# Kernel tuning notes

Hardware: AMD Instinct MI355X
Metric: run time of the kernel (lower is better)

## Reference

```python
import jax, jax.numpy as jnp
import numpy as np

NUM_NODES = 100000
NUM_EDGES = 1600000
NUM_GRAPHS = 64
IN_DIM, HID, NCLS = 64, 128, 10


def setup_inputs() -> dict:
    key = jax.random.key(0)
    ks = jax.random.split(key, 12)
    x = jax.random.normal(ks[0], (NUM_NODES, IN_DIM), dtype=jnp.float32)
    src = jax.random.randint(ks[1], (NUM_EDGES,), 0, NUM_NODES, dtype=jnp.int32)
    dst = jax.random.randint(ks[2], (NUM_EDGES,), 0, NUM_NODES, dtype=jnp.int32)
    batch = jnp.sort(jax.random.randint(ks[3], (NUM_NODES,), 0, NUM_GRAPHS, dtype=jnp.int32))
    def glorot(k, shape):
        lim = (6.0 / (shape[0] + shape[1])) ** 0.5
        return jax.random.uniform(k, shape, jnp.float32, -lim, lim)
    return {
        "x": x, "src": src, "dst": dst, "batch": batch,
        "W1": glorot(ks[4], (IN_DIM, HID)), "b1": jnp.zeros((HID,), jnp.float32),
        "W2": glorot(ks[5], (HID, HID)), "b2": jnp.zeros((HID,), jnp.float32),
        "Wl1": glorot(ks[6], (HID, HID // 2)), "bl1": jnp.zeros((HID // 2,), jnp.float32),
        "Wl2": glorot(ks[7], (HID // 2, NCLS)), "bl2": jnp.zeros((NCLS,), jnp.float32),
    }


def gcn_conv(x, W, b, src, dst):
    # GCNConv: out = D^{-1/2} (A + I) D^{-1/2} (x @ W) + b, deg from A+I
    h = x @ W  # [N, H]
    ones = jnp.ones((src.shape[0],), h.dtype)
    deg = jax.ops.segment_sum(ones, dst, num_segments=NUM_NODES) + 1.0  # +1 self-loop
    dinv = jax.lax.rsqrt(deg)  # [N]
    norm = dinv[src] * dinv[dst]  # [E]
    msg = h[src] * norm[:, None]  # [E, H] gather + scale
    agg = jax.ops.segment_sum(msg, dst, num_segments=NUM_NODES)  # scatter-add
    agg = agg + h * (dinv * dinv)[:, None]  # self-loop message
    return agg + b


def reference(x, src, dst, batch, W1, b1, W2, b2, Wl1, bl1, Wl2, bl2):
    h = jax.nn.relu(gcn_conv(x, W1, b1, src, dst))
    h = jax.nn.relu(gcn_conv(h, W2, b2, src, dst))
    # global mean pool per graph
    sums = jax.ops.segment_sum(h, batch, num_segments=NUM_GRAPHS)  # [G, H]
    cnts = jax.ops.segment_sum(jnp.ones((h.shape[0],), h.dtype), batch, num_segments=NUM_GRAPHS)
    pooled = sums / jnp.maximum(cnts, 1.0)[:, None]
    h = jax.nn.relu(pooled @ Wl1 + bl1)
    return h @ Wl2 + bl2  # [G, num_classes]
```

## Files before the change

### kernel.cpp

```cpp
#include <hip/hip_runtime.h>
#include <hip/hip_bf16.h>

#define NODES_N 100000
#define EDGES_E 1600000
#define GRAPHS_G 64

#define BIN_SHIFT 7
#define BIN_NODES 128
#define NBINS 782
#define NB1 1024
#define EPB1 1563

typedef unsigned int uint;
typedef unsigned short ushort;
typedef __attribute__((ext_vector_type(8))) short bf16x8;
typedef __attribute__((ext_vector_type(4))) float f32x4;


__device__ inline uint pack_bf2(float lo, float hi) {
    __hip_bfloat162 h2 = __float22bfloat162_rn(make_float2(lo, hi));
    return *reinterpret_cast<uint*>(&h2);
}

__device__ inline void acc_bf2(uint w, float& a0, float& a1) {
    a0 += __uint_as_float(w << 16);
    a1 += __uint_as_float(w & 0xffff0000u);
}

__device__ inline ushort f2bf(float v) {
    __hip_bfloat16 b = __float2bfloat16(v);
    return *reinterpret_cast<ushort*>(&b);
}


__global__ __launch_bounds__(256) void p1_hist_k(const int* __restrict__ dst,
                                                 int* __restrict__ hist_t) {
    __shared__ int h[NBINS];
    for (int i = threadIdx.x; i < NBINS; i += 256) h[i] = 0;
    __syncthreads();
    int b = blockIdx.x;
    int e0 = b * EPB1, e1 = min(EDGES_E, e0 + EPB1);
    for (int e = e0 + threadIdx.x; e < e1; e += 256)
        atomicAdd(&h[dst[e] >> BIN_SHIFT], 1);
    __syncthreads();
    for (int i = threadIdx.x; i < NBINS; i += 256)
        hist_t[i * NB1 + b] = h[i];
}

__global__ __launch_bounds__(256) void p1_scanbins_k(int* __restrict__ hist_t,
                                                     int* __restrict__ bintot) {
    __shared__ int sd[256];
    __shared__ int carry;
    int bin = blockIdx.x, t = threadIdx.x;
    if (t == 0) carry = 0;
    __syncthreads();
    int* row = hist_t + bin * NB1;
    for (int base = 0; base < NB1; base += 256) {
        int v = row[base + t];
        sd[t] = v; __syncthreads();
        for (int o = 1; o < 256; o <<= 1) {
            int x = (t >= o) ? sd[t - o] : 0;
            __syncthreads();
            sd[t] += x;
            __syncthreads();
        }
        row[base + t] = carry + sd[t] - v;
        __syncthreads();
        if (t == 255) carry += sd[255];
        __syncthreads();
    }
    if (t == 0) bintot[bin] = carry;
}

__global__ __launch_bounds__(256) void binstart_k(const int* __restrict__ bintot,
                                                  int* __restrict__ binstart,
                                                  int* __restrict__ rowptr) {
    __shared__ int sd[256];
    __shared__ int carry;
    int t = threadIdx.x;
    if (t == 0) carry = 0;
    __syncthreads();
    for (int base = 0; base < NBINS; base += 256) {
        int i = base + t;
        int v = (i < NBINS) ? bintot[i] : 0;
        sd[t] = v; __syncthreads();
        for (int o = 1; o < 256; o <<= 1) {
            int x = (t >= o) ? sd[t - o] : 0;
            __syncthreads();
            sd[t] += x;
            __syncthreads();
        }
        if (i < NBINS) binstart[i] = carry + sd[t] - v;
        __syncthreads();
        if (t == 255) carry += sd[255];
        __syncthreads();
    }
    if (t == 0) { binstart[NBINS] = EDGES_E; rowptr[NODES_N] = EDGES_E; }
}

__global__ __launch_bounds__(256) void p1_scatter_k(const int* __restrict__ src,
                                                    const int* __restrict__ dst,
                                                    const int* __restrict__ hist_t,
                                                    const int* __restrict__ binstart,
                                                    uint2* __restrict__ pairs) {
    __shared__ int cur[NBINS];
    int b = blockIdx.x;
    for (int i = threadIdx.x; i < NBINS; i += 256)
        cur[i] = binstart[i] + hist_t[i * NB1 + b];
    __syncthreads();
    int e0 = b * EPB1, e1 = min(EDGES_E, e0 + EPB1);
    for (int e = e0 + threadIdx.x; e < e1; e += 256) {
        int d = dst[e];
        int pos = atomicAdd(&cur[d >> BIN_SHIFT], 1);
        pairs[pos] = make_uint2((uint)src[e], (uint)d);
    }
}

__global__ __launch_bounds__(256) void p2_build_k(const uint2* __restrict__ pairs,
                                                  const int* __restrict__ binstart,
                                                  int* __restrict__ colidx,
                                                  int* __restrict__ rowptr,
                                                  int* __restrict__ deg) {
    __shared__ int h[BIN_NODES];
    __shared__ int off[BIN_NODES];
    __shared__ int cur[BIN_NODES];
    int bin = blockIdx.x, t = threadIdx.x;
    int node0 = bin << BIN_SHIFT;
    if (t < BIN_NODES) h[t] = 0;
    __syncthreads();
    int e0 = binstart[bin], e1 = binstart[bin + 1];
    for (int e = e0 + t; e < e1; e += 256)
        atomicAdd(&h[pairs[e].y & (BIN_NODES - 1)], 1);
    __syncthreads();
    if (t < BIN_NODES) off[t] = h[t];
    __syncthreads();
    for (int o = 1; o < BIN_NODES; o <<= 1) {
        int x = (t < BIN_NODES && t >= o) ? off[t - o] : 0;
        __syncthreads();
        if (t < BIN_NODES) off[t] += x;
        __syncthreads();
    }
    if (t < BIN_NODES) {
        int excl = off[t] - h[t];
        cur[t] = e0 + excl;
        int node = node0 + t;
        if (node < NODES_N) {
            rowptr[node] = e0 + excl;
            deg[node] = h[t];
        }
    }
    __syncthreads();
    for (int e = e0 + t; e < e1; e += 256) {
        uint2 p = pairs[e];
        int pos = atomicAdd(&cur[p.y & (BIN_NODES - 1)], 1);
        colidx[pos] = (int)p.x;
    }
}

__global__ void dinv_k(const int* __restrict__ deg, int n, float* __restrict__ dinv) {
    int i = blockIdx.x * blockDim.x + threadIdx.x;
    if (i < n) dinv[i] = rsqrtf((float)deg[i] + 1.0f);
}


__global__ __launch_bounds__(256) void scale_x_k(const float* __restrict__ x,
                                                 const float* __restrict__ dinv,
                                                 uint* __restrict__ xt, int n) {
    int gid = blockIdx.x * blockDim.x + threadIdx.x;
    if (gid >= n * 8) return;
    int row = gid >> 3, l = gid & 7;
    float dv = dinv[row];
    const float* p = &x[(size_t)row * 64 + l * 8];
    float4 a = *(const float4*)p;
    float4 b = *(const float4*)(p + 4);
    uint4 o;
    o.x = pack_bf2(a.x * dv, a.y * dv);
    o.y = pack_bf2(a.z * dv, a.w * dv);
    o.z = pack_bf2(b.x * dv, b.y * dv);
    o.w = pack_bf2(b.z * dv, b.w * dv);
    *(uint4*)&xt[(size_t)row * 32 + l * 4] = o;
}


__global__ __launch_bounds__(256) void gather64_k(const uint* __restrict__ xt,
                                                  const int* __restrict__ rowptr,
                                                  const int* __restrict__ colidx,
                                                  uint* __restrict__ st, int n) {
    int lane = threadIdx.x & 7;
    int local = threadIdx.x >> 3;
    int co = lane * 4;
    for (int node = blockIdx.x * 32 + local; node < n; node += gridDim.x * 32) {
        float a0=0,a1=0,a2=0,a3=0,a4=0,a5=0,a6=0,a7=0;
        uint4 v = *(const uint4*)&xt[(size_t)node * 32 + co];
        acc_bf2(v.x, a0, a1); acc_bf2(v.y, a2, a3);
        acc_bf2(v.z, a4, a5); acc_bf2(v.w, a6, a7);
        int beg = rowptr[node], end = rowptr[node + 1];
        int e = beg;
        for (; e + 3 < end; e += 4) {
            int s0 = colidx[e], s1 = colidx[e+1], s2 = colidx[e+2], s3 = colidx[e+3];
            uint4 v0 = *(const uint4*)&xt[(size_t)s0 * 32 + co];
            uint4 v1 = *(const uint4*)&xt[(size_t)s1 * 32 + co];
            uint4 v2 = *(const uint4*)&xt[(size_t)s2 * 32 + co];
            uint4 v3 = *(const uint4*)&xt[(size_t)s3 * 32 + co];
            acc_bf2(v0.x,a0,a1); acc_bf2(v0.y,a2,a3); acc_bf2(v0.z,a4,a5); acc_bf2(v0.w,a6,a7);
            acc_bf2(v1.x,a0,a1); acc_bf2(v1.y,a2,a3); acc_bf2(v1.z,a4,a5); acc_bf2(v1.w,a6,a7);
            acc_bf2(v2.x,a0,a1); acc_bf2(v2.y,a2,a3); acc_bf2(v2.z,a4,a5); acc_bf2(v2.w,a6,a7);
            acc_bf2(v3.x,a0,a1); acc_bf2(v3.y,a2,a3); acc_bf2(v3.z,a4,a5); acc_bf2(v3.w,a6,a7);
        }
        for (; e < end; e++) {
            uint4 v0 = *(const uint4*)&xt[(size_t)colidx[e] * 32 + co];
            acc_bf2(v0.x,a0,a1); acc_bf2(v0.y,a2,a3); acc_bf2(v0.z,a4,a5); acc_bf2(v0.w,a6,a7);
        }
        uint4 o;
        o.x = pack_bf2(a0, a1);
        o.y = pack_bf2(a2, a3);
        o.z = pack_bf2(a4, a5);
        o.w = pack_bf2(a6, a7);
        *(uint4*)&st[(size_t)node * 32 + co] = o;
    }
}


__global__ __launch_bounds__(256) void gather128_k(const uint* __restrict__ hp,
                                                   const int* __restrict__ rowptr,
                                                   const int* __restrict__ colidx,
                                                   const float* __restrict__ dinv,
                                                   const float* __restrict__ bias,
                                                   uint* __restrict__ h2b, int n) {
    int lane = threadIdx.x & 15;
    int local = threadIdx.x >> 4;
    int co = lane * 4;
    for (int node = blockIdx.x * 16 + local; node < n; node += gridDim.x * 16) {
        float a0=0,a1=0,a2=0,a3=0,a4=0,a5=0,a6=0,a7=0;
        uint4 v = *(const uint4*)&hp[(size_t)node * 64 + co];
        acc_bf2(v.x, a0, a1); acc_bf2(v.y, a2, a3);
        acc_bf2(v.z, a4, a5); acc_bf2(v.w, a6, a7);
        int beg = rowptr[node], end = rowptr[node + 1];
        int e = beg;
        for (; e + 3 < end; e += 4) {
            int s0 = colidx[e], s1 = colidx[e+1], s2 = colidx[e+2], s3 = colidx[e+3];
            uint4 v0 = *(const uint4*)&hp[(size_t)s0 * 64 + co];
            uint4 v1 = *(const uint4*)&hp[(size_t)s1 * 64 + co];
            uint4 v2 = *(const uint4*)&hp[(size_t)s2 * 64 + co];
            uint4 v3 = *(const uint4*)&hp[(size_t)s3 * 64 + co];
            acc_bf2(v0.x,a0,a1); acc_bf2(v0.y,a2,a3); acc_bf2(v0.z,a4,a5); acc_bf2(v0.w,a6,a7);
            acc_bf2(v1.x,a0,a1); acc_bf2(v1.y,a2,a3); acc_bf2(v1.z,a4,a5); acc_bf2(v1.w,a6,a7);
            acc_bf2(v2.x,a0,a1); acc_bf2(v2.y,a2,a3); acc_bf2(v2.z,a4,a5); acc_bf2(v2.w,a6,a7);
            acc_bf2(v3.x,a0,a1); acc_bf2(v3.y,a2,a3); acc_bf2(v3.z,a4,a5); acc_bf2(v3.w,a6,a7);
        }
        for (; e < end; e++) {
            uint4 v0 = *(const uint4*)&hp[(size_t)colidx[e] * 64 + co];
            acc_bf2(v0.x,a0,a1); acc_bf2(v0.y,a2,a3); acc_bf2(v0.z,a4,a5); acc_bf2(v0.w,a6,a7);
        }
        float dv = dinv[node];
        int jb = lane * 8;
        float4 b0 = *(const float4*)&bias[jb];
        float4 b1 = *(const float4*)&bias[jb + 4];
        float o0 = fmaxf(fmaf(dv, a0, b0.x), 0.f);
        float o1 = fmaxf(fmaf(dv, a1, b0.y), 0.f);
        float o2 = fmaxf(fmaf(dv, a2, b0.z), 0.f);
        float o3 = fmaxf(fmaf(dv, a3, b0.w), 0.f);
        float o4 = fmaxf(fmaf(dv, a4, b1.x), 0.f);
        float o5 = fmaxf(fmaf(dv, a5, b1.y), 0.f);
        float o6 = fmaxf(fmaf(dv, a6, b1.z), 0.f);
        float o7 = fmaxf(fmaf(dv, a7, b1.w), 0.f);
        uint4 ov;
        ov.x = pack_bf2(o0, o1);
        ov.y = pack_bf2(o2, o3);
        ov.z = pack_bf2(o4, o5);
        ov.w = pack_bf2(o6, o7);
        *(uint4*)&h2b[(size_t)node * 64 + co] = ov;
    }
}


template <int K>
__global__ void pack_w_k(const float* __restrict__ W, ushort* __restrict__ Wf) {
    constexpr int KS = K / 32;
    int gid = blockIdx.x * 256 + threadIdx.x;
    if (gid >= 8 * KS * 512) return;
    int j = gid & 7, l = (gid >> 3) & 63, f = gid >> 9;
    int nt = f / KS, ks = f - nt * KS;
    int k = ks * 32 + ((l >> 4) & 3) * 8 + j;
    int n = nt * 16 + (l & 15);
    Wf[gid] = f2bf(W[k * 128 + n]);
}


template <int K, int EPI>
__global__ __launch_bounds__(256) void gemm_mfma_k(const ushort* __restrict__ A,
                                                   const ushort* __restrict__ Wf,
                                                   const float* __restrict__ dinv,
                                                   const float* __restrict__ bias,
                                                   ushort* __restrict__ outb, int n) {
    constexpr int KS = K / 32;
    int wave = threadIdx.x >> 6;
    int lane = threadIdx.x & 63;
    int row0 = (blockIdx.x * 4 + wave) * 16;
    if (row0 >= n) return;
    int m = lane & 15, g = lane >> 4;
    int arow = min(row0 + m, n - 1);

    bf16x8 a[KS];
    const ushort* abase = &A[(size_t)arow * K + g * 8];
#pragma unroll
    for (int ks = 0; ks < KS; ks++)
        a[ks] = *reinterpret_cast<const bf16x8*>(abase + ks * 32);

    f32x4 acc[8];
#pragma unroll
    for (int nt = 0; nt < 8; nt++) {
        acc[nt] = (f32x4){0.f, 0.f, 0.f, 0.f};
#pragma unroll
        for (int ks = 0; ks < KS; ks++) {
            bf16x8 b = *reinterpret_cast<const bf16x8*>(&Wf[((size_t)(nt * KS + ks) * 64 + lane) * 8]);
            acc[nt] = __builtin_amdgcn_mfma_f32_16x16x32_bf16(a[ks], b, acc[nt], 0, 0, 0);
        }
    }

    int orow0 = row0 + g * 4;
#pragma unroll
    for (int r = 0; r < 4; r++) {
        int row = orow0 + r;
        if (row < n) {
            float dvr = dinv[row];
#pragma unroll
            for (int nt = 0; nt < 8; nt++) {
                float v = acc[nt][r] * dvr;
                if (EPI == 0) v = fmaxf(v + bias[nt * 16 + m], 0.f);
                outb[(size_t)row * 128 + nt * 16 + m] = f2bf(v);
            }
        }
    }
}


__global__ __launch_bounds__(128) void pool_k(const uint* __restrict__ h2b,
                                              const int* __restrict__ batch, int n,
                                              float* __restrict__ sums, float* __restrict__ cnts) {
    int j = threadIdx.x;
    int wj = j >> 1;
    int hi = j & 1;
    int chunk = (n + gridDim.x - 1) / gridDim.x;
    int i0 = blockIdx.x * chunk;
    int i1 = min(n, i0 + chunk);
    if (i0 >= n) return;
    int cur = batch[i0];
    float acc = 0.f;
    int cnt = 0;
    for (int i = i0; i < i1; i++) {
        int g = batch[i];
        if (g != cur) {
            atomicAdd(&sums[cur * 128 + j], acc);
            if (j == 0) atomicAdd(&cnts[cur], (float)cnt);
            acc = 0.f; cnt = 0; cur = g;
        }
        uint w = h2b[(size_t)i * 64 + wj];
        acc += __uint_as_float(hi ? (w & 0xffff0000u) : (w << 16));
        cnt++;
    }
    atomicAdd(&sums[cur * 128 + j], acc);
    if (j == 0) atomicAdd(&cnts[cur], (float)cnt);
}


__global__ __launch_bounds__(64) void mlp_k(const float* __restrict__ sums, const float* __restrict__ cnts,
                                            const float* __restrict__ Wl1, const float* __restrict__ bl1,
                                            const float* __restrict__ Wl2, const float* __restrict__ bl2,
                                            float* __restrict__ out) {
    __shared__ float pooled[128];
    __shared__ float hidden[64];
    int g = blockIdx.x, t = threadIdx.x;
    float c = fmaxf(cnts[g], 1.0f);
    pooled[t]      = sums[g * 128 + t] / c;
    pooled[t + 64] = sums[g * 128 + 64 + t] / c;
    __syncthreads();
    float a = bl1[t];
#pragma unroll 4
    for (int cc = 0; cc < 128; cc++) a = fmaf(pooled[cc], Wl1[cc * 64 + t], a);
    hidden[t] = fmaxf(a, 0.f);
    __syncthreads();
    if (t < 10) {
        float o = bl2[t];
#pragma unroll 8
        for (int jj = 0; jj < 64; jj++) o = fmaf(hidden[jj], Wl2[jj * 10 + t], o);
        out[g * 10 + t] = o;
    }
}


extern "C" void kernel_launch(void* const* d_in, const int* in_sizes, int n_in,
                              void* d_out, int out_size, void* d_ws, size_t ws_size,
                              hipStream_t stream) {
    const float* x    = (const float*)d_in[0];
    const int*   src  = (const int*)d_in[1];
    const int*   dst  = (const int*)d_in[2];
    const int*   batch= (const int*)d_in[3];
    const float* W1   = (const float*)d_in[4];
    const float* b1   = (const float*)d_in[5];
    const float* W2   = (const float*)d_in[6];
    const float* b2   = (const float*)d_in[7];
    const float* Wl1  = (const float*)d_in[8];
    const float* bl1  = (const float*)d_in[9];
    const float* Wl2  = (const float*)d_in[10];
    const float* bl2  = (const float*)d_in[11];
    float* out = (float*)d_out;

    const int N = NODES_N;

    size_t off = 0;
    auto take = [&](size_t bytes) { size_t o = off; off = (off + bytes + 255) & ~(size_t)255; return o; };
    char* ws = (char*)d_ws;
    ushort* h1b  = (ushort*)(ws + take((size_t)N * 128 * 2));
    uint*   h2p  = (uint*)(ws + take((size_t)N * 128 * 2));
    size_t  shbytes = (size_t)EDGES_E * 8;
    char*   shreg = ws + take(shbytes);
    uint2*  pairs = (uint2*)shreg;
    uint*   stil  = (uint*)shreg;
    uint*   xt   = (uint*)(ws + take((size_t)N * 64 * 2));
    float*  dinv = (float*)(ws + take((size_t)N * 4));
    ushort* W1f  = (ushort*)(ws + take((size_t)64 * 128 * 2));
    ushort* W2f  = (ushort*)(ws + take((size_t)128 * 128 * 2));
    size_t zbytes = ((size_t)GRAPHS_G * 128 + GRAPHS_G) * 4;
    char*  zbase  = ws + take(zbytes);
    float* sums   = (float*)zbase;
    float* cnts   = (float*)(zbase + (size_t)GRAPHS_G * 128 * 4);
    int*   rowptr = (int*)(ws + take((size_t)(N + 1) * 4));
    int*   deg    = (int*)(ws + take((size_t)N * 4));
    int*   colidx = (int*)(ws + take((size_t)EDGES_E * 4));
    int*   hist_t = (int*)(ws + take((size_t)NBINS * NB1 * 4));
    int*   bintot = (int*)(ws + take((size_t)NBINS * 4));
    int*   binstart = (int*)(ws + take((size_t)(NBINS + 1) * 4));
    uint*  h2b = (uint*)h1b;
    (void)ws_size; (void)in_sizes; (void)n_in; (void)out_size;

    hipMemsetAsync(zbase, 0, zbytes, stream);

    pack_w_k<64><<<(64 * 128 + 255) / 256, 256, 0, stream>>>(W1, W1f);
    pack_w_k<128><<<(128 * 128 + 255) / 256, 256, 0, stream>>>(W2, W2f);

    p1_hist_k<<<NB1, 256, 0, stream>>>(dst, hist_t);
    p1_scanbins_k<<<NBINS, 256, 0, stream>>>(hist_t, bintot);
    binstart_k<<<1, 256, 0, stream>>>(bintot, binstart, rowptr);
    p1_scatter_k<<<NB1, 256, 0, stream>>>(src, dst, hist_t, binstart, pairs);
    p2_build_k<<<NBINS, 256, 0, stream>>>(pairs, binstart, colidx, rowptr, deg);
    dinv_k<<<(N + 255) / 256, 256, 0, stream>>>(deg, N, dinv);

    scale_x_k<<<(N * 8 + 255) / 256, 256, 0, stream>>>(x, dinv, xt, N);
    gather64_k<<<2048, 256, 0, stream>>>(xt, rowptr, colidx, stil, N);
    int gblk = (N + 63) / 64;
    gemm_mfma_k<64, 0><<<gblk, 256, 0, stream>>>((const ushort*)stil, W1f, dinv, b1, h1b, N);

    gemm_mfma_k<128, 1><<<gblk, 256, 0, stream>>>(h1b, W2f, dinv, nullptr, (ushort*)h2p, N);
    gather128_k<<<2048, 256, 0, stream>>>(h2p, rowptr, colidx, dinv, b2, h2b, N);

    pool_k<<<1024, 128, 0, stream>>>(h2b, batch, N, sums, cnts);
    mlp_k<<<GRAPHS_G, 64, 0, stream>>>(sums, cnts, Wl1, bl1, Wl2, bl2, out);
}
```

Baseline: 252.9 us.

## Pack edge pairs to 32 bits, fuse small kernels, split 128-wide gather

The CSR build now packs each (src, dst-within-bin) edge into a single 32-bit word instead of a uint2, and computes dinv directly inside p2_build. This halves the pair-buffer traffic and removes the separate deg array and dinv kernel. It also halves the first-pass block count, replaces the chunked bin scan with one 1024-thread scan, and merges the two weight-packing kernels into one launch. The 128-wide second-layer gather is split into two launches, each handling 64 columns, so each pass touches a smaller feature footprint that may stay in cache. The cost is reading the CSR structure twice and adding an extra launch.

```diff
diff --git a/kernel.cpp b/kernel.cpp
--- a/kernel.cpp
+++ b/kernel.cpp
@@ -8,8 +8,8 @@
 #define BIN_SHIFT 7
 #define BIN_NODES 128
 #define NBINS 782
-#define NB1 1024
-#define EPB1 1563
+#define NB1 512
+#define EPB1 3125
 
 typedef unsigned int uint;
 typedef unsigned short ushort;
@@ -72,29 +72,20 @@
     if (t == 0) bintot[bin] = carry;
 }
 
-__global__ __launch_bounds__(256) void binstart_k(const int* __restrict__ bintot,
-                                                  int* __restrict__ binstart,
-                                                  int* __restrict__ rowptr) {
-    __shared__ int sd[256];
-    __shared__ int carry;
+__global__ __launch_bounds__(1024) void binstart_k(const int* __restrict__ bintot,
+                                                   int* __restrict__ binstart,
+                                                   int* __restrict__ rowptr) {
+    __shared__ int sd[1024];
     int t = threadIdx.x;
-    if (t == 0) carry = 0;
-    __syncthreads();
-    for (int base = 0; base < NBINS; base += 256) {
-        int i = base + t;
-        int v = (i < NBINS) ? bintot[i] : 0;
-        sd[t] = v; __syncthreads();
-        for (int o = 1; o < 256; o <<= 1) {
-            int x = (t >= o) ? sd[t - o] : 0;
-            __syncthreads();
-            sd[t] += x;
-            __syncthreads();
-        }
-        if (i < NBINS) binstart[i] = carry + sd[t] - v;
-        __syncthreads();
-        if (t == 255) carry += sd[255];
-        __syncthreads();
-    }
+    int v = (t < NBINS) ? bintot[t] : 0;
+    sd[t] = v; __syncthreads();
+    for (int o = 1; o < 1024; o <<= 1) {
+        int x = (t >= o) ? sd[t - o] : 0;
+        __syncthreads();
+        sd[t] += x;
+        __syncthreads();
+    }
+    if (t < NBINS) binstart[t] = sd[t] - v;
     if (t == 0) { binstart[NBINS] = EDGES_E; rowptr[NODES_N] = EDGES_E; }
 }
 
@@ -102,7 +93,7 @@
                                                     const int* __restrict__ dst,
                                                     const int* __restrict__ hist_t,
                                                     const int* __restrict__ binstart,
-                                                    uint2* __restrict__ pairs) {
+                                                    uint* __restrict__ pairs) {
     __shared__ int cur[NBINS];
     int b = blockIdx.x;
     for (int i = threadIdx.x; i < NBINS; i += 256)
@@ -112,15 +103,15 @@
     for (int e = e0 + threadIdx.x; e < e1; e += 256) {
         int d = dst[e];
         int pos = atomicAdd(&cur[d >> BIN_SHIFT], 1);
-        pairs[pos] = make_uint2((uint)src[e], (uint)d);
-    }
-}
-
-__global__ __launch_bounds__(256) void p2_build_k(const uint2* __restrict__ pairs,
+        pairs[pos] = ((uint)src[e] << BIN_SHIFT) | (uint)(d & (BIN_NODES - 1));
+    }
+}
+
+__global__ __launch_bounds__(256) void p2_build_k(const uint* __restrict__ pairs,
                                                   const int* __restrict__ binstart,
                                                   int* __restrict__ colidx,
                                                   int* __restrict__ rowptr,
-                                                  int* __restrict__ deg) {
+                                                  float* __restrict__ dinv) {
     __shared__ int h[BIN_NODES];
     __shared__ int off[BIN_NODES];
     __shared__ int cur[BIN_NODES];
@@ -130,7 +121,7 @@
     __syncthreads();
     int e0 = binstart[bin], e1 = binstart[bin + 1];
     for (int e = e0 + t; e < e1; e += 256)
-        atomicAdd(&h[pairs[e].y & (BIN_NODES - 1)], 1);
+        atomicAdd(&h[pairs[e] & (BIN_NODES - 1)], 1);
     __syncthreads();
     if (t < BIN_NODES) off[t] = h[t];
     __syncthreads();
@@ -146,20 +137,15 @@
         int node = node0 + t;
         if (node < NODES_N) {
             rowptr[node] = e0 + excl;
-            deg[node] = h[t];
+            dinv[node] = rsqrtf((float)h[t] + 1.0f);
         }
     }
     __syncthreads();
     for (int e = e0 + t; e < e1; e += 256) {
-        uint2 p = pairs[e];
-        int pos = atomicAdd(&cur[p.y & (BIN_NODES - 1)], 1);
-        colidx[pos] = (int)p.x;
-    }
-}
-
-__global__ void dinv_k(const int* __restrict__ deg, int n, float* __restrict__ dinv) {
-    int i = blockIdx.x * blockDim.x + threadIdx.x;
-    if (i < n) dinv[i] = rsqrtf((float)deg[i] + 1.0f);
+        uint p = pairs[e];
+        int pos = atomicAdd(&cur[p & (BIN_NODES - 1)], 1);
+        colidx[pos] = (int)(p >> BIN_SHIFT);
+    }
 }
 
 
@@ -221,16 +207,17 @@
 }
 
 
+template <int P>
 __global__ __launch_bounds__(256) void gather128_k(const uint* __restrict__ hp,
                                                    const int* __restrict__ rowptr,
                                                    const int* __restrict__ colidx,
                                                    const float* __restrict__ dinv,
                                                    const float* __restrict__ bias,
                                                    uint* __restrict__ h2b, int n) {
-    int lane = threadIdx.x & 15;
-    int local = threadIdx.x >> 4;
-    int co = lane * 4;
-    for (int node = blockIdx.x * 16 + local; node < n; node += gridDim.x * 16) {
+    int lane = threadIdx.x & 7;
+    int local = threadIdx.x >> 3;
+    int co = P * 32 + lane * 4;
+    for (int node = blockIdx.x * 32 + local; node < n; node += gridDim.x * 32) {
         float a0=0,a1=0,a2=0,a3=0,a4=0,a5=0,a6=0,a7=0;
         uint4 v = *(const uint4*)&hp[(size_t)node * 64 + co];
         acc_bf2(v.x, a0, a1); acc_bf2(v.y, a2, a3);
@@ -253,7 +240,7 @@
             acc_bf2(v0.x,a0,a1); acc_bf2(v0.y,a2,a3); acc_bf2(v0.z,a4,a5); acc_bf2(v0.w,a6,a7);
         }
         float dv = dinv[node];
-        int jb = lane * 8;
+        int jb = P * 64 + lane * 8;
         float4 b0 = *(const float4*)&bias[jb];
         float4 b1 = *(const float4*)&bias[jb + 4];
         float o0 = fmaxf(fmaf(dv, a0, b0.x), 0.f);
@@ -274,16 +261,19 @@
 }
 
 
-template <int K>
-__global__ void pack_w_k(const float* __restrict__ W, ushort* __restrict__ Wf) {
-    constexpr int KS = K / 32;
-    int gid = blockIdx.x * 256 + threadIdx.x;
-    if (gid >= 8 * KS * 512) return;
+__device__ inline void pack_w_one(const float* W, ushort* Wf, int gid, int KS) {
     int j = gid & 7, l = (gid >> 3) & 63, f = gid >> 9;
     int nt = f / KS, ks = f - nt * KS;
     int k = ks * 32 + ((l >> 4) & 3) * 8 + j;
     int n = nt * 16 + (l & 15);
     Wf[gid] = f2bf(W[k * 128 + n]);
+}
+
+__global__ void pack_w_both_k(const float* __restrict__ W1, ushort* __restrict__ W1f,
+                              const float* __restrict__ W2, ushort* __restrict__ W2f) {
+    int gid = blockIdx.x * 256 + threadIdx.x;
+    if (gid < 8192) pack_w_one(W1, W1f, gid, 2);
+    else if (gid < 8192 + 16384) pack_w_one(W2, W2f, gid - 8192, 4);
 }
 
 
@@ -413,9 +403,9 @@
     char* ws = (char*)d_ws;
     ushort* h1b  = (ushort*)(ws + take((size_t)N * 128 * 2));
     uint*   h2p  = (uint*)(ws + take((size_t)N * 128 * 2));
-    size_t  shbytes = (size_t)EDGES_E * 8;
+    size_t  shbytes = (size_t)N * 64 * 2;
     char*   shreg = ws + take(shbytes);
-    uint2*  pairs = (uint2*)shreg;
+    uint*   pairs = (uint*)shreg;
     uint*   stil  = (uint*)shreg;
     uint*   xt   = (uint*)(ws + take((size_t)N * 64 * 2));
     float*  dinv = (float*)(ws + take((size_t)N * 4));
@@ -426,7 +416,6 @@
     float* sums   = (float*)zbase;
     float* cnts   = (float*)(zbase + (size_t)GRAPHS_G * 128 * 4);
     int*   rowptr = (int*)(ws + take((size_t)(N + 1) * 4));
-    int*   deg    = (int*)(ws + take((size_t)N * 4));
     int*   colidx = (int*)(ws + take((size_t)EDGES_E * 4));
     int*   hist_t = (int*)(ws + take((size_t)NBINS * NB1 * 4));
     int*   bintot = (int*)(ws + take((size_t)NBINS * 4));
@@ -436,15 +425,13 @@
 
     hipMemsetAsync(zbase, 0, zbytes, stream);
 
-    pack_w_k<64><<<(64 * 128 + 255) / 256, 256, 0, stream>>>(W1, W1f);
-    pack_w_k<128><<<(128 * 128 + 255) / 256, 256, 0, stream>>>(W2, W2f);
+    pack_w_both_k<<<(8192 + 16384 + 255) / 256, 256, 0, stream>>>(W1, W1f, W2, W2f);
 
     p1_hist_k<<<NB1, 256, 0, stream>>>(dst, hist_t);
     p1_scanbins_k<<<NBINS, 256, 0, stream>>>(hist_t, bintot);
-    binstart_k<<<1, 256, 0, stream>>>(bintot, binstart, rowptr);
+    binstart_k<<<1, 1024, 0, stream>>>(bintot, binstart, rowptr);
     p1_scatter_k<<<NB1, 256, 0, stream>>>(src, dst, hist_t, binstart, pairs);
-    p2_build_k<<<NBINS, 256, 0, stream>>>(pairs, binstart, colidx, rowptr, deg);
-    dinv_k<<<(N + 255) / 256, 256, 0, stream>>>(deg, N, dinv);
+    p2_build_k<<<NBINS, 256, 0, stream>>>(pairs, binstart, colidx, rowptr, dinv);
 
     scale_x_k<<<(N * 8 + 255) / 256, 256, 0, stream>>>(x, dinv, xt, N);
     gather64_k<<<2048, 256, 0, stream>>>(xt, rowptr, colidx, stil, N);
@@ -452,7 +439,9 @@
     gemm_mfma_k<64, 0><<<gblk, 256, 0, stream>>>((const ushort*)stil, W1f, dinv, b1, h1b, N);
 
     gemm_mfma_k<128, 1><<<gblk, 256, 0, stream>>>(h1b, W2f, dinv, nullptr, (ushort*)h2p, N);
-    gather128_k<<<2048, 256, 0, stream>>>(h2p, rowptr, colidx, dinv, b2, h2b, N);
+    int g128 = (N + 31) / 32;
+    gather128_k<0><<<g128, 256, 0, stream>>>(h2p, rowptr, colidx, dinv, b2, h2b, N);
+    gather128_k<1><<<g128, 256, 0, stream>>>(h2p, rowptr, colidx, dinv, b2, h2b, N);
 
     pool_k<<<1024, 128, 0, stream>>>(h2b, batch, N, sums, cnts);
     mlp_k<<<GRAPHS_G, 64, 0, stream>>>(sums, cnts, Wl1, bl1, Wl2, bl2, out);
```

After: 236.9 us. -6.3%, faster.
